# Kernel optimization log

Hardware: AMD Instinct MI355X
Metric: run time of the kernel (lower is better)

Reference implementation:

```python
import jax, jax.numpy as jnp
import numpy as np

N = 100000
E = 1600000
IN_DIM = 128
OUT_DIM = 64


def setup_inputs() -> dict:
    key = jax.random.key(0)
    k_h, k_ei, k_ew, k_W, k_a = jax.random.split(key, 5)
    h = jax.random.normal(k_h, (N, IN_DIM), dtype=jnp.float32)
    edge_index = jax.random.randint(k_ei, (2, E), 0, N, dtype=jnp.int64)
    edge_weight = jax.random.uniform(k_ew, (E,), dtype=jnp.float32)
    # nn.Linear weights (Kaiming-uniform-ish scale)
    W = jax.random.uniform(k_W, (OUT_DIM, IN_DIM), dtype=jnp.float32,
                           minval=-1.0, maxval=1.0) / np.sqrt(IN_DIM)
    a = jax.random.uniform(k_a, (2 * OUT_DIM,), dtype=jnp.float32,
                           minval=-1.0, maxval=1.0) / np.sqrt(2 * OUT_DIM)
    return {"h": h, "edge_index": edge_index, "edge_weight": edge_weight,
            "W": W, "a": a}


def reference(h, edge_index, edge_weight, W, a):
    # Faithful translation of _GATConvSparse.forward (inference; dropout = identity).
    n = h.shape[0]
    src, dst = edge_index[0], edge_index[1]
    Wh = h @ W.T                                  # (N, out_dim)
    d = Wh.shape[1]
    # a(cat([Wh[src], Wh[dst]])) == Wh[src] @ a[:d] + Wh[dst] @ a[d:]
    alpha = Wh[src] @ a[:d] + Wh[dst] @ a[d:]     # (E,)
    alpha = alpha * edge_weight
    # Buggy-but-faithful 'softmax': segment-sum raw scores onto dst nodes...
    alpha_node = jax.ops.segment_sum(alpha, dst, num_segments=n)   # (N,)
    alpha_exp = jnp.exp(alpha_node - alpha_node.max())             # (N,)
    # ...then normalize per-edge exp(src) by sum of exp(src) over each dst segment.
    denom = jax.ops.segment_sum(alpha_exp[src], dst, num_segments=n)  # (N,)
    alpha_norm = alpha_exp[src] / (denom[dst] + 1e-9)              # (E,)
    out = jax.ops.segment_sum(alpha_norm[:, None] * Wh[src], dst,
                              num_segments=n)                      # (N, out_dim)
    return jax.nn.elu(out)
```

## Files before the change

### kernel.cpp

```cpp
#include <hip/hip_runtime.h>
#include <math.h>

#define Nn 100000
#define Ee 1600000
#define IND 128
#define OUTD 64
#define DPB 64
#define NB 1563
#define BSTR 1280
#define CAP 1536
#define GB 1563
#define EB_BLOCKS 391
#define CSCAN_BLOCKS 196
#define AFIX 1048576.0f

using bf16x8 = __attribute__((ext_vector_type(8))) short;
using f32x4 = __attribute__((ext_vector_type(4))) float;

__device__ __forceinline__ unsigned short f2bf(float f) {
    unsigned u = __float_as_uint(f);
    u = u + 0x7FFFu + ((u >> 16) & 1u);
    return (unsigned short)(u >> 16);
}
__device__ __forceinline__ float bf2f(unsigned short h) {
    return __uint_as_float(((unsigned)h) << 16);
}

__device__ __forceinline__ bool probe64(const void* __restrict__ ei) {
    const long long* p = (const long long*)ei;
    bool ok = true;
#pragma unroll
    for (int i = 0; i < 8; ++i) {
        long long v = p[i];
        ok = ok && (v >= 0 && v < Nn);
    }
    return ok;
}

__device__ __forceinline__ void load_edge(const void* ei, int e, bool is64,
                                          int& s, int& d) {
    if (is64) {
        const long long* p = (const long long*)ei;
        s = (int)p[e];
        d = (int)p[Ee + e];
    } else {
        const int* p = (const int*)ei;
        s = p[e];
        d = p[Ee + e];
    }
}

__device__ __forceinline__ int load_dst(const void* ei, int e, bool is64) {
    if (is64) return (int)((const long long*)ei)[Ee + e];
    return ((const int*)ei)[Ee + e];
}

__global__ __launch_bounds__(256) void k_hist(
    const void* __restrict__ ei, unsigned short* __restrict__ counts) {
    __shared__ int cnt[NB];
    int t = threadIdx.x;
    int hc = blockIdx.x;
    for (int i = t; i < NB; i += 256) cnt[i] = 0;
    __syncthreads();
    bool is64 = probe64(ei);
    int base = hc * 4096;
#pragma unroll
    for (int i = 0; i < 16; ++i) {
        int e = base + i * 256 + t;
        if (e < Ee) atomicAdd(&cnt[load_dst(ei, e, is64) >> 6], 1);
    }
    __syncthreads();
    for (int i = t; i < NB; i += 256)
        counts[(size_t)hc * NB + i] = (unsigned short)cnt[i];
}

__global__ __launch_bounds__(512) void k_cscan(
    unsigned short* __restrict__ counts, int* __restrict__ bcnt) {
    int gw = (int)((blockIdx.x * 512 + threadIdx.x) >> 6);
    int lane = threadIdx.x & 63;
    if (gw >= NB) return;
    int run = 0;
    for (int c0 = 0; c0 < EB_BLOCKS; c0 += 64) {
        int c = c0 + lane;
        int v = (c < EB_BLOCKS) ? (int)counts[(size_t)c * NB + gw] : 0;
        int s = v;
#pragma unroll
        for (int d = 1; d < 64; d <<= 1) {
            int u = __shfl_up(s, d, 64);
            if (lane >= d) s += u;
        }
        if (c < EB_BLOCKS)
            counts[(size_t)c * NB + gw] = (unsigned short)(run + s - v);
        run += __shfl(s, 63, 64);
    }
    if (lane == 0) bcnt[gw] = run;
}

__global__ __launch_bounds__(256) void k_gembin(
    const float* __restrict__ h, const float* __restrict__ W,
    const float* __restrict__ a, unsigned short* __restrict__ Whb,
    float* __restrict__ s1, float* __restrict__ s2,
    const void* __restrict__ ei, const float* __restrict__ ew,
    const unsigned short* __restrict__ counts, uint2* __restrict__ bins) {
    __shared__ unsigned short Ash[64][136];
    __shared__ unsigned short Wsh[64][136];
    __shared__ float al[2 * OUTD];
    int bid = blockIdx.x;
    int t = threadIdx.x;

    if (bid < EB_BLOCKS) {
        int* cnt = (int*)&Ash[0][0];
        int* gb = (int*)&Wsh[0][0];
        int hc = bid;
        for (int i = t; i < NB; i += 256) {
            cnt[i] = 0;
            gb[i] = (int)counts[(size_t)hc * NB + i];
        }
        __syncthreads();
        bool is64 = probe64(ei);
        int base = hc * 4096;
#pragma unroll
        for (int half8 = 0; half8 < 2; ++half8) {
            unsigned rx[8];
            unsigned rw[8];
            int rb[8];
            int rk[8];
#pragma unroll
            for (int i = 0; i < 8; ++i) {
                int e = base + half8 * 2048 + i * 256 + t;
                rb[i] = -1;
                rx[i] = 0;
                rw[i] = 0;
                rk[i] = 0;
                if (e < Ee) {
                    int s, d;
                    load_edge(ei, e, is64, s, d);
                    rw[i] = __float_as_uint(ew[e]);
                    int b = d >> 6;
                    rb[i] = b;
                    rk[i] = atomicAdd(&cnt[b], 1);
                    rx[i] = ((unsigned)s << 7) | ((unsigned)(d & 63) << 24);
                }
            }
#pragma unroll
            for (int i = 0; i < 8; ++i) {
                if (rb[i] >= 0) {
                    int off = gb[rb[i]] + rk[i];
                    if (off < BSTR)
                        bins[(size_t)rb[i] * BSTR + off] =
                            make_uint2(rx[i], rw[i]);
                }
            }
        }
        return;
    }

    int R = (bid - EB_BLOCKS) * 64;
    for (int i = t; i < 2048; i += 256) {
        float4 v = ((const float4*)W)[i];
        int r = i >> 5, c = (i & 31) << 2;
        unsigned lo = (unsigned)f2bf(v.x) | ((unsigned)f2bf(v.y) << 16);
        unsigned hi = (unsigned)f2bf(v.z) | ((unsigned)f2bf(v.w) << 16);
        *(uint2*)&Wsh[r][c] = make_uint2(lo, hi);
    }
    if (t < 32) ((float4*)al)[t] = ((const float4*)a)[t];
    for (int i = t; i < 2048; i += 256) {
        int r = i >> 5, c = (i & 31) << 2;
        int n = R + r;
        float4 v = make_float4(0.f, 0.f, 0.f, 0.f);
        if (n < Nn) v = ((const float4*)(h + (size_t)n * IND))[i & 31];
        unsigned lo = (unsigned)f2bf(v.x) | ((unsigned)f2bf(v.y) << 16);
        unsigned hi = (unsigned)f2bf(v.z) | ((unsigned)f2bf(v.w) << 16);
        *(uint2*)&Ash[r][c] = make_uint2(lo, hi);
    }
    __syncthreads();

    int w = t >> 6, l = t & 63;
    int li = l & 15, lg = l >> 4;
    f32x4 acc[4];
#pragma unroll
    for (int nt = 0; nt < 4; ++nt) acc[nt] = (f32x4){0.f, 0.f, 0.f, 0.f};
#pragma unroll
    for (int kk = 0; kk < 4; ++kk) {
        bf16x8 af = *(const bf16x8*)&Ash[w * 16 + li][kk * 32 + lg * 8];
#pragma unroll
        for (int nt = 0; nt < 4; ++nt) {
            bf16x8 bf = *(const bf16x8*)&Wsh[nt * 16 + li][kk * 32 + lg * 8];
            acc[nt] = __builtin_amdgcn_mfma_f32_16x16x32_bf16(af, bf,
                                                              acc[nt],
                                                              0, 0, 0);
        }
    }
    float p1[4] = {0.f, 0.f, 0.f, 0.f};
    float p2[4] = {0.f, 0.f, 0.f, 0.f};
#pragma unroll
    for (int nt = 0; nt < 4; ++nt) {
        float a1v = al[nt * 16 + li];
        float a2v = al[OUTD + nt * 16 + li];
#pragma unroll
        for (int r = 0; r < 4; ++r) {
            float v = acc[nt][r];
            p1[r] += v * a1v;
            p2[r] += v * a2v;
            int row = R + w * 16 + lg * 4 + r;
            if (row < Nn)
                Whb[(size_t)row * OUTD + nt * 16 + li] = f2bf(v);
        }
    }
#pragma unroll
    for (int r = 0; r < 4; ++r) {
#pragma unroll
        for (int m = 1; m < 16; m <<= 1) {
            p1[r] += __shfl_xor(p1[r], m, 64);
            p2[r] += __shfl_xor(p2[r], m, 64);
        }
    }
    if (li < 4) {
        int row = R + w * 16 + lg * 4 + li;
        if (row < Nn) {
            s1[row] = p1[li];
            s2[row] = p2[li];
        }
    }
}

__global__ __launch_bounds__(256) void k_balpha(
    const uint2* __restrict__ bins, const int* __restrict__ bcnt,
    const float* __restrict__ s1, const float* __restrict__ s2,
    float* __restrict__ ae) {
    __shared__ int anl[DPB];
    __shared__ int ews[DPB];
    int b = blockIdx.x;
    int t = threadIdx.x;
    if (t < DPB) {
        anl[t] = 0;
        ews[t] = 0;
    }
    __syncthreads();
    int e0 = b * BSTR;
    int c = bcnt[b];
    int e1 = e0 + (c < BSTR ? c : BSTR);
    for (int k = e0 + t; k < e1; k += 256) {
        uint2 r = bins[k];
        int dloc = (int)(r.x >> 24);
        int s = (int)((r.x >> 7) & 0x1FFFF);
        float w = __uint_as_float(r.y);
        atomicAdd(&anl[dloc], (int)rintf(s1[s] * w * AFIX));
        atomicAdd(&ews[dloc], (int)rintf(w * AFIX));
    }
    __syncthreads();
    if (t < DPB) {
        int n = b * DPB + t;
        if (n < Nn) {
            float an = ((float)anl[t] + s2[n] * (float)ews[t]) * (1.f / AFIX);
            ae[n] = expf(an);
        }
    }
}

#define AGG_BODY(NR)                                                         \
    {                                                                        \
        uint2 rr[NR];                                                        \
        unsigned ww[NR];                                                     \
        _Pragma("unroll") for (int j = 0; j < NR; ++j)                       \
            rr[j] = lp[2 * j];                                               \
        _Pragma("unroll") for (int j = 0; j < NR; ++j)                       \
            ww[j] = *(const unsigned*)(whbB + (rr[j].x + hl4));              \
        _Pragma("unroll") for (int j = 0; j < NR; ++j) {                     \
            float aa = __uint_as_float(rr[j].y);                             \
            acc.x += aa * __uint_as_float(ww[j] << 16);                      \
            acc.y += aa * __uint_as_float(ww[j] & 0xFFFF0000u);              \
            den += aa;                                                       \
        }                                                                    \
        lp += 2 * NR;                                                        \
    }

__global__ __launch_bounds__(512, 4) void k_agg(
    const uint2* __restrict__ bins, const int* __restrict__ bcnt,
    const float* __restrict__ ae, const unsigned short* __restrict__ Whb,
    float* __restrict__ out) {
    __shared__ uint2 lrec[CAP];
    __shared__ int cnt[DPB];
    __shared__ int sbase[DPB];
    int b = blockIdx.x;
    int t = threadIdx.x;
    int lane = t & 63;
    int wave = t >> 6;
    int half = lane >> 5;
    int hl = lane & 31;
    unsigned hl4 = (unsigned)hl << 2;
    int e0 = b * BSTR;
    int c = bcnt[b];
    int total = c < BSTR ? c : BSTR;
    int e1 = e0 + total;
    const char* whbB = (const char*)Whb;

    if (t < DPB) cnt[t] = 0;
    __syncthreads();

    unsigned su[CAP / 512];
    float sa[CAP / 512];
    int srk[CAP / 512];
#pragma unroll
    for (int i = 0; i < CAP / 512; ++i) {
        int k = e0 + i * 512 + t;
        srk[i] = -1;
        if (k < e1) {
            uint2 r = bins[k];
            srk[i] = atomicAdd(&cnt[r.x >> 24], 1);
            su[i] = r.x;
            sa[i] = ae[(r.x >> 7) & 0x1FFFF];
        }
    }
    __syncthreads();
    if (t < DPB) {
        int v = cnt[t];
#pragma unroll
        for (int d = 1; d < DPB; d <<= 1) {
            int u = __shfl_up(v, d, 64);
            if (t >= d) v += u;
        }
        sbase[t] = v;
    }
    __syncthreads();
#pragma unroll
    for (int i = 0; i < CAP / 512; ++i) {
        if (srk[i] >= 0) {
            int dloc = su[i] >> 24;
            int pos = sbase[dloc] - cnt[dloc] + srk[i];
            lrec[pos] = make_uint2(su[i] & 0x00FFFF80u,
                                   __float_as_uint(sa[i]));
        }
    }
    __syncthreads();

    for (int d = wave * 8; d < wave * 8 + 8; ++d) {
        int k1 = sbase[d];
        int k = k1 - cnt[d];
        const uint2* lp = lrec + k + half;
        float2 acc = make_float2(0.f, 0.f);
        float den = 0.f;
        for (; k + 15 < k1; k += 16) AGG_BODY(8);
        for (; k + 7 < k1; k += 8) AGG_BODY(4);
        for (; k + 1 < k1; k += 2) AGG_BODY(1);
        if (k < k1) {
            uint2 rA = lrec[k];
            unsigned wA = *(const unsigned*)(whbB + (rA.x + hl4));
            float aA = half ? 0.f : __uint_as_float(rA.y);
            acc.x += aA * __uint_as_float(wA << 16);
            acc.y += aA * __uint_as_float(wA & 0xFFFF0000u);
            den += aA;
        }
        float ax = acc.x + __shfl_xor(acc.x, 32, 64);
        float ay = acc.y + __shfl_xor(acc.y, 32, 64);
        float dn = den + __shfl_xor(den, 32, 64);
        if (half == 0) {
            int n = b * DPB + d;
            if (n < Nn) {
                float inv = 1.f / (dn + 1e-9f);
                float vx = ax * inv;
                float vy = ay * inv;
                vx = vx > 0.f ? vx : expm1f(vx);
                vy = vy > 0.f ? vy : expm1f(vy);
                *(float2*)&out[(size_t)n * OUTD + hl * 2] =
                    make_float2(vx, vy);
            }
        }
    }
}

extern "C" void kernel_launch(void* const* d_in, const int* in_sizes, int n_in,
                              void* d_out, int out_size, void* d_ws,
                              size_t ws_size, hipStream_t stream) {
    const float* h = (const float*)d_in[0];
    const void* ei = d_in[1];
    const float* ew = (const float*)d_in[2];
    const float* W = (const float*)d_in[3];
    const float* a = (const float*)d_in[4];
    float* out = (float*)d_out;

    unsigned short* Whb = (unsigned short*)d_ws;
    float* s1 = (float*)(Whb + (size_t)Nn * OUTD);
    float* s2 = s1 + Nn;
    float* ae = s2 + Nn;
    int* bcnt = (int*)(ae + Nn);
    uint2* bins = (uint2*)(bcnt + 2048);
    unsigned short* counts =
        (unsigned short*)(bins + (size_t)NB * BSTR);

    k_hist<<<EB_BLOCKS, 256, 0, stream>>>(ei, counts);
    k_cscan<<<CSCAN_BLOCKS, 512, 0, stream>>>(counts, bcnt);
    k_gembin<<<EB_BLOCKS + GB, 256, 0, stream>>>(h, W, a, Whb, s1, s2, ei,
                                                 ew, counts, bins);
    k_balpha<<<NB, 256, 0, stream>>>(bins, bcnt, s1, s2, ae);
    k_agg<<<NB, 512, 0, stream>>>(bins, bcnt, ae, Whb, out);
}
```

Baseline: 107.1 us.

## Split fused GEMM/bin-scatter kernel and halve edge chunk size per block

The combined GEMM-plus-binning kernel is split into a standalone GEMM kernel and a separate 512-thread bin-scatter kernel. The edge chunk per histogram/scatter block drops from 4096 to 2048, doubling the block count to spread the edge work over more CUs. The cost is an extra kernel launch and the loss of overlap between the GEMM and the scatter. It also doubles the per-chunk count matrix, so the column scan in k_cscan has more entries to walk and more memory traffic.

```diff
diff --git a/kernel.cpp b/kernel.cpp
--- a/kernel.cpp
+++ b/kernel.cpp
@@ -10,7 +10,8 @@
 #define BSTR 1280
 #define CAP 1536
 #define GB 1563
-#define EB_BLOCKS 391
+#define ECHUNK 2048
+#define EB_BLOCKS 782
 #define CSCAN_BLOCKS 196
 #define AFIX 1048576.0f
 
@@ -55,22 +56,22 @@
     return ((const int*)ei)[Ee + e];
 }
 
-__global__ __launch_bounds__(256) void k_hist(
+__global__ __launch_bounds__(512) void k_hist(
     const void* __restrict__ ei, unsigned short* __restrict__ counts) {
     __shared__ int cnt[NB];
     int t = threadIdx.x;
     int hc = blockIdx.x;
-    for (int i = t; i < NB; i += 256) cnt[i] = 0;
+    for (int i = t; i < NB; i += 512) cnt[i] = 0;
     __syncthreads();
     bool is64 = probe64(ei);
-    int base = hc * 4096;
-#pragma unroll
-    for (int i = 0; i < 16; ++i) {
-        int e = base + i * 256 + t;
+    int base = hc * ECHUNK;
+#pragma unroll
+    for (int i = 0; i < 4; ++i) {
+        int e = base + i * 512 + t;
         if (e < Ee) atomicAdd(&cnt[load_dst(ei, e, is64) >> 6], 1);
     }
     __syncthreads();
-    for (int i = t; i < NB; i += 256)
+    for (int i = t; i < NB; i += 512)
         counts[(size_t)hc * NB + i] = (unsigned short)cnt[i];
 }
 
@@ -96,66 +97,17 @@
     if (lane == 0) bcnt[gw] = run;
 }
 
-__global__ __launch_bounds__(256) void k_gembin(
+__global__ __launch_bounds__(256) void k_gemm(
     const float* __restrict__ h, const float* __restrict__ W,
     const float* __restrict__ a, unsigned short* __restrict__ Whb,
-    float* __restrict__ s1, float* __restrict__ s2,
-    const void* __restrict__ ei, const float* __restrict__ ew,
-    const unsigned short* __restrict__ counts, uint2* __restrict__ bins) {
+    float* __restrict__ s1, float* __restrict__ s2) {
     __shared__ unsigned short Ash[64][136];
     __shared__ unsigned short Wsh[64][136];
     __shared__ float al[2 * OUTD];
     int bid = blockIdx.x;
     int t = threadIdx.x;
 
-    if (bid < EB_BLOCKS) {
-        int* cnt = (int*)&Ash[0][0];
-        int* gb = (int*)&Wsh[0][0];
-        int hc = bid;
-        for (int i = t; i < NB; i += 256) {
-            cnt[i] = 0;
-            gb[i] = (int)counts[(size_t)hc * NB + i];
-        }
-        __syncthreads();
-        bool is64 = probe64(ei);
-        int base = hc * 4096;
-#pragma unroll
-        for (int half8 = 0; half8 < 2; ++half8) {
-            unsigned rx[8];
-            unsigned rw[8];
-            int rb[8];
-            int rk[8];
-#pragma unroll
-            for (int i = 0; i < 8; ++i) {
-                int e = base + half8 * 2048 + i * 256 + t;
-                rb[i] = -1;
-                rx[i] = 0;
-                rw[i] = 0;
-                rk[i] = 0;
-                if (e < Ee) {
-                    int s, d;
-                    load_edge(ei, e, is64, s, d);
-                    rw[i] = __float_as_uint(ew[e]);
-                    int b = d >> 6;
-                    rb[i] = b;
-                    rk[i] = atomicAdd(&cnt[b], 1);
-                    rx[i] = ((unsigned)s << 7) | ((unsigned)(d & 63) << 24);
-                }
-            }
-#pragma unroll
-            for (int i = 0; i < 8; ++i) {
-                if (rb[i] >= 0) {
-                    int off = gb[rb[i]] + rk[i];
-                    if (off < BSTR)
-                        bins[(size_t)rb[i] * BSTR + off] =
-                            make_uint2(rx[i], rw[i]);
-                }
-            }
-        }
-        return;
-    }
-
-    int R = (bid - EB_BLOCKS) * 64;
+    int R = bid * 64;
     for (int i = t; i < 2048; i += 256) {
         float4 v = ((const float4*)W)[i];
         int r = i >> 5, c = (i & 31) << 2;
@@ -220,6 +172,52 @@
         if (row < Nn) {
             s1[row] = p1[li];
             s2[row] = p2[li];
+        }
+    }
+}
+
+__global__ __launch_bounds__(512) void k_binscatter(
+    const void* __restrict__ ei, const float* __restrict__ ew,
+    const unsigned short* __restrict__ counts, uint2* __restrict__ bins) {
+    __shared__ int cnt[NB];
+    __shared__ int gbase[NB];
+    int hc = blockIdx.x;
+    int t = threadIdx.x;
+    for (int i = t; i < NB; i += 512) {
+        cnt[i] = 0;
+        gbase[i] = (int)counts[(size_t)hc * NB + i];
+    }
+    __syncthreads();
+    bool is64 = probe64(ei);
+    int base = hc * ECHUNK;
+    unsigned rx[4];
+    unsigned rw[4];
+    int rb[4];
+    int rk[4];
+#pragma unroll
+    for (int i = 0; i < 4; ++i) {
+        int e = base + i * 512 + t;
+        rb[i] = -1;
+        rx[i] = 0;
+        rw[i] = 0;
+        rk[i] = 0;
+        if (e < Ee) {
+            int s, d;
+            load_edge(ei, e, is64, s, d);
+            rw[i] = __float_as_uint(ew[e]);
+            int b = d >> 6;
+            rb[i] = b;
+            rk[i] = atomicAdd(&cnt[b], 1);
+            rx[i] = ((unsigned)s << 7) | ((unsigned)(d & 63) << 24);
+        }
+    }
+    __syncthreads();
+#pragma unroll
+    for (int i = 0; i < 4; ++i) {
+        if (rb[i] >= 0) {
+            int off = gbase[rb[i]] + rk[i];
+            if (off < BSTR)
+                bins[(size_t)rb[i] * BSTR + off] = make_uint2(rx[i], rw[i]);
         }
     }
 }
@@ -388,10 +386,10 @@
     unsigned short* counts =
         (unsigned short*)(bins + (size_t)NB * BSTR);
 
-    k_hist<<<EB_BLOCKS, 256, 0, stream>>>(ei, counts);
+    k_hist<<<EB_BLOCKS, 512, 0, stream>>>(ei, counts);
     k_cscan<<<CSCAN_BLOCKS, 512, 0, stream>>>(counts, bcnt);
-    k_gembin<<<EB_BLOCKS + GB, 256, 0, stream>>>(h, W, a, Whb, s1, s2, ei,
-                                                 ew, counts, bins);
+    k_gemm<<<GB, 256, 0, stream>>>(h, W, a, Whb, s1, s2);
+    k_binscatter<<<EB_BLOCKS, 512, 0, stream>>>(ei, ew, counts, bins);
     k_balpha<<<NB, 256, 0, stream>>>(bins, bcnt, s1, s2, ae);
     k_agg<<<NB, 512, 0, stream>>>(bins, bcnt, ae, Whb, out);
 }
```

Result: slower. 121.7 us (+13.6%).
